# Kernel tuning notes

Hardware: AMD Instinct MI355X
Metric: run time of the kernel (lower is better)

The kernel has to match this reference:

```python
import jax, jax.numpy as jnp
import numpy as np

BN_EPS = 1e-5


def setup_inputs() -> dict:
    key = jax.random.key(0)
    ks = jax.random.split(key, 12)
    B, N, G, D = 16, 8192, 64, 384
    C_IN = D + 64 + 3  # 451
    inp = {
        "features": jax.random.normal(ks[0], (B, G, D), jnp.float32),
        "centers": jax.random.normal(ks[1], (B, G, 3), jnp.float32),
        "pc": jax.random.normal(ks[2], (B, N, 3), jnp.float32),
        "category": jax.random.randint(ks[3], (B,), 0, 16, jnp.int64),
        "cat_embed": jax.random.normal(ks[4], (16, 64), jnp.float32) * 0.02,
        "w1": jax.random.normal(ks[5], (256, C_IN), jnp.float32) * (1.0 / np.sqrt(C_IN)),
        "b1": jnp.zeros((256,), jnp.float32),
        "g1": jnp.ones((256,), jnp.float32),
        "be1": jnp.zeros((256,), jnp.float32),
        "m1": jnp.zeros((256,), jnp.float32),
        "v1": jnp.ones((256,), jnp.float32),
        "w2": jax.random.normal(ks[6], (256, 256), jnp.float32) * (1.0 / 16.0),
        "b2": jnp.zeros((256,), jnp.float32),
        "g2": jnp.ones((256,), jnp.float32),
        "be2": jnp.zeros((256,), jnp.float32),
        "m2": jnp.zeros((256,), jnp.float32),
        "v2": jnp.ones((256,), jnp.float32),
        "w3": jax.random.normal(ks[7], (50, 256), jnp.float32) * (1.0 / 16.0),
        "b3": jnp.zeros((50,), jnp.float32),
    }
    return inp


def _bn(x, g, be, m, v):  # x: [B, N, C], inference-mode BatchNorm1d
    return (x - m) * (g * jax.lax.rsqrt(v + BN_EPS)) + be


def reference(features, centers, pc, category, cat_embed,
              w1, b1, g1, be1, m1, v1,
              w2, b2, g2, be2, m2, v2,
              w3, b3):
    B, N, _ = pc.shape
    # Euclidean cdist via norm expansion: [B, N, G]
    p2 = jnp.sum(pc * pc, axis=-1, keepdims=True)            # [B,N,1]
    c2 = jnp.sum(centers * centers, axis=-1)[:, None, :]     # [B,1,G]
    dot = jnp.einsum('bnd,bgd->bng', pc, centers)
    dist = jnp.sqrt(jnp.clip(p2 + c2 - 2.0 * dot, 1e-12))
    # top-3 smallest
    neg_d, knn_idx = jax.lax.top_k(-dist, 3)                 # [B,N,3]
    knn_dist = -neg_d
    w = 1.0 / (knn_dist + 1e-8)
    w = w / jnp.sum(w, axis=-1, keepdims=True)               # [B,N,3]
    # gather per-batch: features [B,G,D], knn_idx [B,N,3] -> [B,N,3,D]
    knn_features = jax.vmap(lambda f, i: f[i])(features, knn_idx)
    point_features = jnp.einsum('bnkd,bnk->bnd', knn_features, w)  # [B,N,D]
    cat_feat = jnp.broadcast_to(cat_embed[category][:, None, :], (B, N, 64))
    combined = jnp.concatenate([point_features, cat_feat, pc], axis=-1)  # [B,N,451]
    # Conv1d(k=1) == per-point dense layer; keep [B,N,C] layout
    h = jnp.einsum('bnc,oc->bno', combined, w1) + b1
    h = jax.nn.relu(_bn(h, g1, be1, m1, v1))
    h = jnp.einsum('bnc,oc->bno', h, w2) + b2
    h = jax.nn.relu(_bn(h, g2, be2, m2, v2))
    seg_logits = jnp.einsum('bnc,oc->bno', h, w3) + b3       # [B,N,50]
    return seg_logits
```

## Files before the change

### kernel.cpp

```cpp
#include <hip/hip_runtime.h>

#define TPB 256

typedef unsigned short u16;
typedef unsigned int u32;
typedef short short8 __attribute__((ext_vector_type(8)));
typedef float f32x4 __attribute__((ext_vector_type(4)));

#define KEEP(x) asm volatile("" :: "v"(x))

__device__ __forceinline__ u16 f2bf(float x) {
  union { float f; u32 u; } v;
  v.f = x;
  u32 r = v.u + 0x7FFFu + ((v.u >> 16) & 1u);
  return (u16)(r >> 16);
}

__device__ __forceinline__ float bf2f(u16 x) {
  union { u32 u; float f; } v;
  v.u = ((u32)x) << 16;
  return v.f;
}

__global__ void prep_kernel(const float* __restrict__ w1, const float* __restrict__ b1,
                            const float* __restrict__ g1, const float* __restrict__ be1,
                            const float* __restrict__ m1, const float* __restrict__ v1,
                            const float* __restrict__ w2, const float* __restrict__ b2,
                            const float* __restrict__ g2, const float* __restrict__ be2,
                            const float* __restrict__ m2, const float* __restrict__ v2,
                            const float* __restrict__ w3, const float* __restrict__ b3,
                            u16* __restrict__ w1b, u16* __restrict__ w2b, u16* __restrict__ w3b,
                            float* __restrict__ b1p, float* __restrict__ b2p, float* __restrict__ b3p)
{
  int i = blockIdx.x * TPB + threadIdx.x;
  if (i < 256 * 480) {
    int o = i / 480;
    int k = i - o * 480;
    float s = g1[o] * rsqrtf(v1[o] + 1e-5f);
    u16 r = 0;
    if (k < 451) r = f2bf(w1[o * 451 + k] * s);
    w1b[i] = r;
  }
  if (i < 256 * 256) {
    int o = i >> 8;
    float s = g2[o] * rsqrtf(v2[o] + 1e-5f);
    w2b[i] = f2bf(w2[i] * s);
  }
  if (i < 64 * 256) {
    int o = i >> 8;
    u16 r = 0;
    if (o < 50) r = f2bf(w3[i]);
    w3b[i] = r;
  }
  if (i < 256) {
    float s1 = g1[i] * rsqrtf(v1[i] + 1e-5f);
    b1p[i] = (b1[i] - m1[i]) * s1 + be1[i];
    float s2 = g2[i] * rsqrtf(v2[i] + 1e-5f);
    b2p[i] = (b2[i] - m2[i]) * s2 + be2[i];
  }
  if (i < 64) {
    b3p[i] = (i < 50) ? b3[i] : 0.f;
  }
}

__global__ __launch_bounds__(512, 2)
void gcalc_kernel(const float* __restrict__ features, const int* __restrict__ category,
                  const float* __restrict__ cat_embed, const u16* __restrict__ w1b,
                  const float* __restrict__ b1p,
                  u16* __restrict__ G, float* __restrict__ bias1)
{
  __shared__ u16 Fs[64 * 392];
  const int b    = blockIdx.x >> 1;
  const int och0 = (blockIdx.x & 1) * 128;
  const int tid  = threadIdx.x;
  const int lane = tid & 63;
  const int wv   = tid >> 6;
  const int lr   = lane & 15;
  const int lk   = (lane >> 4) * 8;
  const int r0   = (lane >> 4) * 4;
  const int catv = category[b];

  const f32x4* F4 = (const f32x4*)(features + b * 24576);
  #pragma unroll
  for (int it = 0; it < 12; ++it) {
    int idx = tid + 512 * it;
    int c = idx / 96;
    int d4 = idx - c * 96;
    f32x4 v = F4[c * 96 + d4];
    u32 lo = (u32)f2bf(v[0]) | ((u32)f2bf(v[1]) << 16);
    u32 hi = (u32)f2bf(v[2]) | ((u32)f2bf(v[3]) << 16);
    *(uint2*)&Fs[c * 392 + d4 * 4] = make_uint2(lo, hi);
  }

  if (tid < 128) {
    int o = och0 + tid;
    float acc = b1p[o];
    const u16* wr = w1b + o * 480 + 384;
    const float* ce = cat_embed + catv * 64;
    #pragma unroll 8
    for (int j = 0; j < 64; ++j) acc += bf2f(wr[j]) * ce[j];
    bias1[b * 256 + o] = acc;
    u16* Go = G + (b * 256 + o) * 96;
    Go[64] = wr[64]; Go[65] = wr[65]; Go[66] = wr[66];
    #pragma unroll
    for (int k = 67; k < 96; ++k) Go[k] = 0;
  }
  __syncthreads();

  const int ch = och0 + wv * 16 + lr;
  f32x4 acc[4];
  {
    f32x4 z = {0.f, 0.f, 0.f, 0.f};
    #pragma unroll
    for (int m = 0; m < 4; ++m) acc[m] = z;
  }
  #pragma unroll
  for (int ks = 0; ks < 12; ++ks) {
    short8 bv = *(const short8*)(w1b + ch * 480 + ks * 32 + lk);
    #pragma unroll
    for (int m = 0; m < 4; ++m) {
      short8 av = *(const short8*)(&Fs[(m * 16 + lr) * 392 + ks * 32 + lk]);
      acc[m] = __builtin_amdgcn_mfma_f32_16x16x32_bf16(av, bv, acc[m], 0, 0, 0);
    }
  }
  #pragma unroll
  for (int m = 0; m < 4; ++m)
    #pragma unroll
    for (int r = 0; r < 4; ++r)
      G[(b * 256 + ch) * 96 + m * 16 + r0 + r] = f2bf(acc[m][r]);
}

#define LDP 104
#define LDH 264

__global__ __launch_bounds__(512, 4)
void fused_kernel(const float* __restrict__ centers, const float* __restrict__ pc,
                  const u16* __restrict__ G, const float* __restrict__ bias1,
                  const u16* __restrict__ w2b, const u16* __restrict__ w3b,
                  const float* __restrict__ b2p, const float* __restrict__ b3p,
                  float* __restrict__ out)
{
  __shared__ u16 hbuf[128 * LDH];
  __shared__ float centl[192];
  __shared__ float pcl[384];

  const int bx   = blockIdx.x;
  const int b    = bx >> 6;
  const int n0   = (bx & 63) << 7;
  const int tid  = threadIdx.x;
  const int lane = tid & 63;
  const int wv   = tid >> 6;
  const int lr   = lane & 15;
  const int lk   = (lane >> 4) * 8;
  const int r0   = (lane >> 4) * 4;

  u16*   Pm   = hbuf;
  float* scrd = (float*)((char*)hbuf + 32768);
  int*   scri = (int*)((char*)hbuf + 40960);

  short8 bvG[3][2];
  #pragma unroll
  for (int ks = 0; ks < 3; ++ks)
    #pragma unroll
    for (int n = 0; n < 2; ++n)
      bvG[ks][n] = *(const short8*)(G + (b * 256 + wv * 32 + n * 16 + lr) * 96 + ks * 32 + lk);

  {
    u32* Pw = (u32*)Pm;
    #pragma unroll
    for (int i = 0; i < 13; ++i) Pw[tid + 512 * i] = 0;
  }
  if (tid < 192) centl[tid] = centers[b * 192 + tid];
  if (tid < 384) pcl[tid] = pc[(b * 8192 + n0) * 3 + tid];
  __syncthreads();

  {
    int p = tid >> 2, c = tid & 3;
    float px = pcl[p * 3 + 0], py = pcl[p * 3 + 1], pz = pcl[p * 3 + 2];
    float p2 = px * px + py * py + pz * pz;
    float bd0 = 3.4e38f, bd1 = 3.4e38f, bd2 = 3.4e38f;
    int bi0 = 0, bi1 = 0, bi2 = 0;
    int j0 = c * 16;
    for (int j = j0; j < j0 + 16; ++j) {
      float cx = centl[j * 3 + 0], cy = centl[j * 3 + 1], cz = centl[j * 3 + 2];
      float dotv = px * cx + py * cy + pz * cz;
      float c2 = cx * cx + cy * cy + cz * cz;
      float d2 = (p2 + c2) - 2.f * dotv;
      if (d2 < bd2) {
        if (d2 < bd1) {
          if (d2 < bd0) { bd2 = bd1; bi2 = bi1; bd1 = bd0; bi1 = bi0; bd0 = d2; bi0 = j; }
          else          { bd2 = bd1; bi2 = bi1; bd1 = d2; bi1 = j; }
        } else          { bd2 = d2; bi2 = j; }
      }
    }
    scrd[tid * 3 + 0] = bd0; scrd[tid * 3 + 1] = bd1; scrd[tid * 3 + 2] = bd2;
    scri[tid * 3 + 0] = bi0; scri[tid * 3 + 1] = bi1; scri[tid * 3 + 2] = bi2;
  }
  __syncthreads();

  if (tid < 128) {
    float bd0 = 3.4e38f, bd1 = 3.4e38f, bd2 = 3.4e38f;
    int bi0 = 0, bi1 = 0, bi2 = 0;
    #pragma unroll
    for (int c = 0; c < 4; ++c) {
      int t = tid * 4 + c;
      #pragma unroll
      for (int s = 0; s < 3; ++s) {
        float d2 = scrd[t * 3 + s];
        int   j  = scri[t * 3 + s];
        if (d2 < bd2) {
          if (d2 < bd1) {
            if (d2 < bd0) { bd2 = bd1; bi2 = bi1; bd1 = bd0; bi1 = bi0; bd0 = d2; bi0 = j; }
            else          { bd2 = bd1; bi2 = bi1; bd1 = d2; bi1 = j; }
          } else          { bd2 = d2; bi2 = j; }
        }
      }
    }
    float dd0 = sqrtf(fmaxf(bd0, 1e-12f));
    float dd1 = sqrtf(fmaxf(bd1, 1e-12f));
    float dd2 = sqrtf(fmaxf(bd2, 1e-12f));
    float u0 = 1.f / (dd0 + 1e-8f);
    float u1 = 1.f / (dd1 + 1e-8f);
    float u2 = 1.f / (dd2 + 1e-8f);
    float inv = 1.f / (u0 + u1 + u2);
    u16* Pr = Pm + tid * LDP;
    Pr[bi0] = f2bf(u0 * inv);
    Pr[bi1] = f2bf(u1 * inv);
    Pr[bi2] = f2bf(u2 * inv);
    Pr[64] = f2bf(pcl[tid * 3 + 0]);
    Pr[65] = f2bf(pcl[tid * 3 + 1]);
    Pr[66] = f2bf(pcl[tid * 3 + 2]);
  }
  KEEP(bvG[0][0]); KEEP(bvG[0][1]); KEEP(bvG[1][0]);
  KEEP(bvG[1][1]); KEEP(bvG[2][0]); KEEP(bvG[2][1]);
  __syncthreads();

  f32x4 acc[8][2];
  {
    f32x4 z = {0.f, 0.f, 0.f, 0.f};
    #pragma unroll
    for (int m = 0; m < 8; ++m) { acc[m][0] = z; acc[m][1] = z; }
  }
  #pragma unroll
  for (int ks = 0; ks < 3; ++ks) {
    short8 av[8];
    #pragma unroll
    for (int m = 0; m < 8; ++m)
      av[m] = *(const short8*)(&Pm[(m * 16 + lr) * LDP + ks * 32 + lk]);
    #pragma unroll
    for (int m = 0; m < 8; ++m)
      #pragma unroll
      for (int n = 0; n < 2; ++n)
        acc[m][n] = __builtin_amdgcn_mfma_f32_16x16x32_bf16(av[m], bvG[ks][n], acc[m][n], 0, 0, 0);
  }
  __syncthreads();

  #pragma unroll
  for (int n = 0; n < 2; ++n) {
    float bb = bias1[b * 256 + wv * 32 + n * 16 + lr];
    #pragma unroll
    for (int m = 0; m < 8; ++m)
      #pragma unroll
      for (int r = 0; r < 4; ++r) {
        float v = acc[m][n][r] + bb;
        v = v > 0.f ? v : 0.f;
        int row = m * 16 + r0 + r;
        int col = (wv * 32 + n * 16 + lr) ^ (((row >> 2) & 7) << 3);
        hbuf[row * LDH + col] = f2bf(v);
      }
  }
  __syncthreads();

  {
    f32x4 z = {0.f, 0.f, 0.f, 0.f};
    #pragma unroll
    for (int m = 0; m < 8; ++m) { acc[m][0] = z; acc[m][1] = z; }
  }
  #pragma unroll
  for (int ks = 0; ks < 8; ++ks) {
    short8 bv[2];
    #pragma unroll
    for (int n = 0; n < 2; ++n)
      bv[n] = *(const short8*)(w2b + (wv * 32 + n * 16 + lr) * 256 + ks * 32 + lk);
    short8 av[8];
    #pragma unroll
    for (int m = 0; m < 8; ++m) {
      int row = m * 16 + lr;
      int g = (ks * 4 + (lane >> 4)) ^ ((row >> 2) & 7);
      av[m] = *(const short8*)(&hbuf[row * LDH + g * 8]);
    }
    #pragma unroll
    for (int m = 0; m < 8; ++m)
      #pragma unroll
      for (int n = 0; n < 2; ++n)
        acc[m][n] = __builtin_amdgcn_mfma_f32_16x16x32_bf16(av[m], bv[n], acc[m][n], 0, 0, 0);
  }
  __syncthreads();

  #pragma unroll
  for (int n = 0; n < 2; ++n) {
    float bb = b2p[wv * 32 + n * 16 + lr];
    #pragma unroll
    for (int m = 0; m < 8; ++m)
      #pragma unroll
      for (int r = 0; r < 4; ++r) {
        float v = acc[m][n][r] + bb;
        v = v > 0.f ? v : 0.f;
        int row = m * 16 + r0 + r;
        int col = (wv * 32 + n * 16 + lr) ^ (((row >> 2) & 7) << 3);
        hbuf[row * LDH + col] = f2bf(v);
      }
  }

  const int wm = wv & 3;
  const int wn = wv >> 2;
  short8 w3f[8][2];
  #pragma unroll
  for (int ks = 0; ks < 8; ++ks)
    #pragma unroll
    for (int j = 0; j < 2; ++j)
      w3f[ks][j] = *(const short8*)(w3b + (wn * 32 + j * 16 + lr) * 256 + ks * 32 + lk);
  #pragma unroll
  for (int ks = 0; ks < 8; ++ks) { KEEP(w3f[ks][0]); KEEP(w3f[ks][1]); }
  __syncthreads();

  {
    f32x4 acc3[2][2];
    f32x4 z = {0.f, 0.f, 0.f, 0.f};
    acc3[0][0] = z; acc3[0][1] = z; acc3[1][0] = z; acc3[1][1] = z;
    #pragma unroll
    for (int ks = 0; ks < 8; ++ks) {
      #pragma unroll
      for (int mi = 0; mi < 2; ++mi) {
        int row = (wm * 2 + mi) * 16 + lr;
        int g = (ks * 4 + (lane >> 4)) ^ ((row >> 2) & 7);
        short8 av = *(const short8*)(&hbuf[row * LDH + g * 8]);
        #pragma unroll
        for (int j = 0; j < 2; ++j)
          acc3[mi][j] = __builtin_amdgcn_mfma_f32_16x16x32_bf16(av, w3f[ks][j], acc3[mi][j], 0, 0, 0);
      }
    }
    #pragma unroll
    for (int j = 0; j < 2; ++j) {
      int c = wn * 32 + j * 16 + lr;
      if (c < 50) {
        float b3v = b3p[c];
        #pragma unroll
        for (int mi = 0; mi < 2; ++mi)
          #pragma unroll
          for (int r = 0; r < 4; ++r) {
            int row = n0 + (wm * 2 + mi) * 16 + r0 + r;
            out[(b * 8192 + row) * 50 + c] = acc3[mi][j][r] + b3v;
          }
      }
    }
  }
}

extern "C" void kernel_launch(void* const* d_in, const int* in_sizes, int n_in,
                              void* d_out, int out_size, void* d_ws, size_t ws_size,
                              hipStream_t stream) {
  const float* features  = (const float*)d_in[0];
  const float* centers   = (const float*)d_in[1];
  const float* pc        = (const float*)d_in[2];
  const int*   category  = (const int*)d_in[3];
  const float* cat_embed = (const float*)d_in[4];
  const float* w1  = (const float*)d_in[5];
  const float* b1  = (const float*)d_in[6];
  const float* g1  = (const float*)d_in[7];
  const float* be1 = (const float*)d_in[8];
  const float* m1  = (const float*)d_in[9];
  const float* v1  = (const float*)d_in[10];
  const float* w2  = (const float*)d_in[11];
  const float* b2  = (const float*)d_in[12];
  const float* g2  = (const float*)d_in[13];
  const float* be2 = (const float*)d_in[14];
  const float* m2  = (const float*)d_in[15];
  const float* v2  = (const float*)d_in[16];
  const float* w3  = (const float*)d_in[17];
  const float* b3  = (const float*)d_in[18];
  float* out = (float*)d_out;

  char* ws = (char*)d_ws;
  u16*   w1b   = (u16*)(ws);
  u16*   w2b   = (u16*)(ws + 245760);
  u16*   w3b   = (u16*)(ws + 376832);
  float* b1p   = (float*)(ws + 409600);
  float* b2p   = (float*)(ws + 410624);
  float* b3p   = (float*)(ws + 411648);
  u16*   G     = (u16*)(ws + 412672);
  float* bias1 = (float*)(ws + 1199104);

  prep_kernel<<<480, TPB, 0, stream>>>(w1, b1, g1, be1, m1, v1,
                                       w2, b2, g2, be2, m2, v2,
                                       w3, b3, w1b, w2b, w3b, b1p, b2p, b3p);
  gcalc_kernel<<<32, 512, 0, stream>>>(features, category, cat_embed, w1b, b1p, G, bias1);

  fused_kernel<<<1024, 512, 0, stream>>>(centers, pc, G, bias1,
                                         w2b, w3b, b2p, b3p, out);
}
```

Measured before the change: 168.5 us.

## Split gcalc across more blocks, prefetch w2 tiles, stage output logits through LDS

Feature bf16 conversion moves into prep_kernel, so gcalc_kernel no longer needs LDS. gcalc now runs as 256 small blocks instead of 32 large ones, giving it more parallelism across CUs. In the fused kernel, the first w2 fragments are loaded before a barrier and register values are pinned across barriers. Output logits are staged in shared memory so stores to the 50-column output are contiguous and coalesced, at the cost of an extra barrier and an LDS round trip.

```diff
diff --git a/kernel.cpp b/kernel.cpp
--- a/kernel.cpp
+++ b/kernel.cpp
@@ -8,6 +8,7 @@
 typedef float f32x4 __attribute__((ext_vector_type(4)));
 
 #define KEEP(x) asm volatile("" :: "v"(x))
+#define PIN(x)  asm volatile("" : "+v"(x))
 
 __device__ __forceinline__ u16 f2bf(float x) {
   union { float f; u32 u; } v;
@@ -29,8 +30,10 @@
                             const float* __restrict__ g2, const float* __restrict__ be2,
                             const float* __restrict__ m2, const float* __restrict__ v2,
                             const float* __restrict__ w3, const float* __restrict__ b3,
+                            const float* __restrict__ features,
                             u16* __restrict__ w1b, u16* __restrict__ w2b, u16* __restrict__ w3b,
-                            float* __restrict__ b1p, float* __restrict__ b2p, float* __restrict__ b3p)
+                            float* __restrict__ b1p, float* __restrict__ b2p, float* __restrict__ b3p,
+                            u16* __restrict__ Fbf)
 {
   int i = blockIdx.x * TPB + threadIdx.x;
   if (i < 256 * 480) {
@@ -61,73 +64,55 @@
   if (i < 64) {
     b3p[i] = (i < 50) ? b3[i] : 0.f;
   }
-}
-
-__global__ __launch_bounds__(512, 2)
-void gcalc_kernel(const float* __restrict__ features, const int* __restrict__ category,
+  if (i < 98304) {
+    f32x4 v = ((const f32x4*)features)[i];
+    u32 lo = (u32)f2bf(v[0]) | ((u32)f2bf(v[1]) << 16);
+    u32 hi = (u32)f2bf(v[2]) | ((u32)f2bf(v[3]) << 16);
+    *(uint2*)&Fbf[i * 4] = make_uint2(lo, hi);
+  }
+}
+
+__global__ __launch_bounds__(256, 8)
+void gcalc_kernel(const u16* __restrict__ Fbf, const int* __restrict__ category,
                   const float* __restrict__ cat_embed, const u16* __restrict__ w1b,
                   const float* __restrict__ b1p,
                   u16* __restrict__ G, float* __restrict__ bias1)
 {
-  __shared__ u16 Fs[64 * 392];
-  const int b    = blockIdx.x >> 1;
-  const int och0 = (blockIdx.x & 1) * 128;
+  const int b    = blockIdx.x >> 4;
+  const int og   = blockIdx.x & 15;
   const int tid  = threadIdx.x;
   const int lane = tid & 63;
   const int wv   = tid >> 6;
   const int lr   = lane & 15;
   const int lk   = (lane >> 4) * 8;
   const int r0   = (lane >> 4) * 4;
-  const int catv = category[b];
-
-  const f32x4* F4 = (const f32x4*)(features + b * 24576);
-  #pragma unroll
-  for (int it = 0; it < 12; ++it) {
-    int idx = tid + 512 * it;
-    int c = idx / 96;
-    int d4 = idx - c * 96;
-    f32x4 v = F4[c * 96 + d4];
-    u32 lo = (u32)f2bf(v[0]) | ((u32)f2bf(v[1]) << 16);
-    u32 hi = (u32)f2bf(v[2]) | ((u32)f2bf(v[3]) << 16);
-    *(uint2*)&Fs[c * 392 + d4 * 4] = make_uint2(lo, hi);
-  }
-
-  if (tid < 128) {
-    int o = och0 + tid;
-    float acc = b1p[o];
+  const u16* Fb  = Fbf + b * 24576;
+  const int ch   = og * 16 + lr;
+
+  f32x4 acc = {0.f, 0.f, 0.f, 0.f};
+  #pragma unroll
+  for (int ks = 0; ks < 12; ++ks) {
+    short8 av = *(const short8*)(Fb + (wv * 16 + lr) * 384 + ks * 32 + lk);
+    short8 bv = *(const short8*)(w1b + ch * 480 + ks * 32 + lk);
+    acc = __builtin_amdgcn_mfma_f32_16x16x32_bf16(av, bv, acc, 0, 0, 0);
+  }
+  #pragma unroll
+  for (int r = 0; r < 4; ++r)
+    G[(b * 256 + ch) * 96 + wv * 16 + r0 + r] = f2bf(acc[r]);
+
+  if (tid < 16) {
+    int o = og * 16 + tid;
     const u16* wr = w1b + o * 480 + 384;
-    const float* ce = cat_embed + catv * 64;
+    const float* ce = cat_embed + category[b] * 64;
+    float a = b1p[o];
     #pragma unroll 8
-    for (int j = 0; j < 64; ++j) acc += bf2f(wr[j]) * ce[j];
-    bias1[b * 256 + o] = acc;
+    for (int j = 0; j < 64; ++j) a += bf2f(wr[j]) * ce[j];
+    bias1[b * 256 + o] = a;
     u16* Go = G + (b * 256 + o) * 96;
     Go[64] = wr[64]; Go[65] = wr[65]; Go[66] = wr[66];
     #pragma unroll
     for (int k = 67; k < 96; ++k) Go[k] = 0;
   }
-  __syncthreads();
-
-  const int ch = och0 + wv * 16 + lr;
-  f32x4 acc[4];
-  {
-    f32x4 z = {0.f, 0.f, 0.f, 0.f};
-    #pragma unroll
-    for (int m = 0; m < 4; ++m) acc[m] = z;
-  }
-  #pragma unroll
-  for (int ks = 0; ks < 12; ++ks) {
-    short8 bv = *(const short8*)(w1b + ch * 480 + ks * 32 + lk);
-    #pragma unroll
-    for (int m = 0; m < 4; ++m) {
-      short8 av = *(const short8*)(&Fs[(m * 16 + lr) * 392 + ks * 32 + lk]);
-      acc[m] = __builtin_amdgcn_mfma_f32_16x16x32_bf16(av, bv, acc[m], 0, 0, 0);
-    }
-  }
-  #pragma unroll
-  for (int m = 0; m < 4; ++m)
-    #pragma unroll
-    for (int r = 0; r < 4; ++r)
-      G[(b * 256 + ch) * 96 + m * 16 + r0 + r] = f2bf(acc[m][r]);
 }
 
 #define LDP 104
@@ -234,6 +219,8 @@
   KEEP(bvG[0][0]); KEEP(bvG[0][1]); KEEP(bvG[1][0]);
   KEEP(bvG[1][1]); KEEP(bvG[2][0]); KEEP(bvG[2][1]);
   __syncthreads();
+  PIN(bvG[0][0]); PIN(bvG[0][1]); PIN(bvG[1][0]);
+  PIN(bvG[1][1]); PIN(bvG[2][0]); PIN(bvG[2][1]);
 
   f32x4 acc[8][2];
   {
@@ -269,7 +256,16 @@
         hbuf[row * LDH + col] = f2bf(v);
       }
   }
-  __syncthreads();
+
+  short8 w2f[2][2];
+  #pragma unroll
+  for (int ks = 0; ks < 2; ++ks)
+    #pragma unroll
+    for (int n = 0; n < 2; ++n)
+      w2f[ks][n] = *(const short8*)(w2b + (wv * 32 + n * 16 + lr) * 256 + ks * 32 + lk);
+  KEEP(w2f[0][0]); KEEP(w2f[0][1]); KEEP(w2f[1][0]); KEEP(w2f[1][1]);
+  __syncthreads();
+  PIN(w2f[0][0]); PIN(w2f[0][1]); PIN(w2f[1][0]); PIN(w2f[1][1]);
 
   {
     f32x4 z = {0.f, 0.f, 0.f, 0.f};
@@ -279,9 +275,12 @@
   #pragma unroll
   for (int ks = 0; ks < 8; ++ks) {
     short8 bv[2];
-    #pragma unroll
-    for (int n = 0; n < 2; ++n)
-      bv[n] = *(const short8*)(w2b + (wv * 32 + n * 16 + lr) * 256 + ks * 32 + lk);
+    if (ks < 2) { bv[0] = w2f[ks][0]; bv[1] = w2f[ks][1]; }
+    else {
+      #pragma unroll
+      for (int n = 0; n < 2; ++n)
+        bv[n] = *(const short8*)(w2b + (wv * 32 + n * 16 + lr) * 256 + ks * 32 + lk);
+    }
     short8 av[8];
     #pragma unroll
     for (int m = 0; m < 8; ++m) {
@@ -323,23 +322,30 @@
   #pragma unroll
   for (int ks = 0; ks < 8; ++ks) { KEEP(w3f[ks][0]); KEEP(w3f[ks][1]); }
   __syncthreads();
-
-  {
-    f32x4 acc3[2][2];
+  #pragma unroll
+  for (int ks = 0; ks < 8; ++ks) { PIN(w3f[ks][0]); PIN(w3f[ks][1]); }
+
+  f32x4 acc3[2][2];
+  {
     f32x4 z = {0.f, 0.f, 0.f, 0.f};
     acc3[0][0] = z; acc3[0][1] = z; acc3[1][0] = z; acc3[1][1] = z;
-    #pragma unroll
-    for (int ks = 0; ks < 8; ++ks) {
-      #pragma unroll
-      for (int mi = 0; mi < 2; ++mi) {
-        int row = (wm * 2 + mi) * 16 + lr;
-        int g = (ks * 4 + (lane >> 4)) ^ ((row >> 2) & 7);
-        short8 av = *(const short8*)(&hbuf[row * LDH + g * 8]);
-        #pragma unroll
-        for (int j = 0; j < 2; ++j)
-          acc3[mi][j] = __builtin_amdgcn_mfma_f32_16x16x32_bf16(av, w3f[ks][j], acc3[mi][j], 0, 0, 0);
-      }
-    }
+  }
+  #pragma unroll
+  for (int ks = 0; ks < 8; ++ks) {
+    #pragma unroll
+    for (int mi = 0; mi < 2; ++mi) {
+      int row = (wm * 2 + mi) * 16 + lr;
+      int g = (ks * 4 + (lane >> 4)) ^ ((row >> 2) & 7);
+      short8 av = *(const short8*)(&hbuf[row * LDH + g * 8]);
+      #pragma unroll
+      for (int j = 0; j < 2; ++j)
+        acc3[mi][j] = __builtin_amdgcn_mfma_f32_16x16x32_bf16(av, w3f[ks][j], acc3[mi][j], 0, 0, 0);
+    }
+  }
+  __syncthreads();
+
+  {
+    float* logb = (float*)hbuf;
     #pragma unroll
     for (int j = 0; j < 2; ++j) {
       int c = wn * 32 + j * 16 + lr;
@@ -349,9 +355,20 @@
         for (int mi = 0; mi < 2; ++mi)
           #pragma unroll
           for (int r = 0; r < 4; ++r) {
-            int row = n0 + (wm * 2 + mi) * 16 + r0 + r;
-            out[(b * 8192 + row) * 50 + c] = acc3[mi][j][r] + b3v;
+            int row = (wm * 2 + mi) * 16 + r0 + r;
+            logb[row * 52 + c] = acc3[mi][j][r] + b3v;
           }
+      }
+    }
+    __syncthreads();
+    float* outb = out + (size_t)(b * 8192 + n0) * 50;
+    #pragma unroll
+    for (int i = 0; i < 13; ++i) {
+      int f = tid + i * 512;
+      if (f < 6400) {
+        int row = (f * 5243) >> 18;
+        int c = f - row * 50;
+        outb[f] = logb[row * 52 + c];
       }
     }
   }
@@ -390,11 +407,13 @@
   float* b3p   = (float*)(ws + 411648);
   u16*   G     = (u16*)(ws + 412672);
   float* bias1 = (float*)(ws + 1199104);
+  u16*   Fbf   = (u16*)(ws + 1215488);
 
   prep_kernel<<<480, TPB, 0, stream>>>(w1, b1, g1, be1, m1, v1,
                                        w2, b2, g2, be2, m2, v2,
-                                       w3, b3, w1b, w2b, w3b, b1p, b2p, b3p);
-  gcalc_kernel<<<32, 512, 0, stream>>>(features, category, cat_embed, w1b, b1p, G, bias1);
+                                       w3, b3, features,
+                                       w1b, w2b, w3b, b1p, b2p, b3p, Fbf);
+  gcalc_kernel<<<256, 256, 0, stream>>>(Fbf, category, cat_embed, w1b, b1p, G, bias1);
 
   fused_kernel<<<1024, 512, 0, stream>>>(centers, pc, G, bias1,
                                          w2b, w3b, b2p, b3p, out);
```

Result: no change. 167.3 us (-0.7%).
